# Optimization experiments

Measured on AMD Instinct MI355X. Metric: run time of the kernel, lower is better.

The kernel has to match this reference:

```python
import jax, jax.numpy as jnp
import numpy as np

N, E, G = 64, 128, 4
D0, ED = 9, 4
H1, H2, H3 = 2000, 500, 100
F1, F2, F3 = 1000, 100, 50


def setup_inputs() -> dict:
    key = jax.random.key(0)
    ks = iter(jax.random.split(key, 32))

    def p(shape, s=0.02):
        return (jax.random.normal(next(ks), shape, jnp.float32) * s)

    inp = {
        "x": jax.random.normal(next(ks), (N, D0), jnp.float32),
        "edge_index": jax.random.randint(next(ks), (2, E), 0, N),
        "edge_attr": jax.random.normal(next(ks), (E, ED), jnp.float32),
        "batch": jnp.sort(jax.random.randint(next(ks), (N,), 0, G)),
        # NNConv layer 1: edge MLP Linear(ED, D0*H1), root weight, bias
        "We1": p((ED, D0 * H1)), "be1": p((D0 * H1,)),
        "root1": p((D0, H1)), "b1": p((H1,)),
        # NNConv layer 2
        "We2": p((ED, H1 * H2)), "be2": p((H1 * H2,)),
        "root2": p((H1, H2)), "b2": p((H2,)),
        # NNConv layer 3
        "We3": p((ED, H2 * H3)), "be3": p((H2 * H3,)),
        "root3": p((H2, H3)), "b3": p((H3,)),
        # FCN head
        "W1": p((H3, F1)), "c1": p((F1,)),
        "W2": p((F1, F2)), "c2": p((F2,)),
        "W3": p((F2, F3)), "c3": p((F3,)),
        "W4": p((F3, 1)), "c4": p((1,)),
    }
    return inp


def _nnconv(x, src, dst, edge_attr, We, be, root, b):
    # edge-conditioned weights: [E, in, out]
    in_dim = x.shape[1]
    w = (edge_attr @ We + be).reshape(edge_attr.shape[0], in_dim, -1)
    # gather source feats, per-edge matmul, scatter-add to targets
    msg = jnp.einsum('ei,eio->eo', x[src], w)
    agg = jax.ops.segment_sum(msg, dst, num_segments=x.shape[0])
    return agg + x @ root + b


def reference(x, edge_index, edge_attr, batch,
              We1, be1, root1, b1,
              We2, be2, root2, b2,
              We3, be3, root3, b3,
              W1, c1, W2, c2, W3, c3, W4, c4):
    src, dst = edge_index[0], edge_index[1]
    h = jax.nn.relu(_nnconv(x, src, dst, edge_attr, We1, be1, root1, b1))
    h = jax.nn.relu(_nnconv(h, src, dst, edge_attr, We2, be2, root2, b2))
    h = jax.nn.relu(_nnconv(h, src, dst, edge_attr, We3, be3, root3, b3))
    # sum readout per graph (dropout layers are identity in eval mode)
    g = jax.ops.segment_sum(h, batch, num_segments=G)  # [G, H3]
    g = jax.nn.relu(g @ W1 + c1)
    g = jax.nn.relu(g @ W2 + c2)
    g = jax.nn.relu(g @ W3 + c3)
    out = g @ W4 + c4
    return out.reshape(-1)  # [G]
```

## Files before the change

### kernel.cpp

```cpp
#include <hip/hip_runtime.h>

#define NN 64
#define EE 128
#define GG 4
#define D0 9
#define EDIM 4
#define H1 2000
#define H2 500
#define H3 100
#define FF1 1000
#define FF2 100
#define FF3 50
#define KDIM 384

#define OFF_A    0
#define OFF_Y    24576
#define OFF_PRE1 28032
#define OFF_PRE2 156032
#define OFF_PRE3 188032
#define OFF_N2   194432
#define OFF_N3   386432
#define OFF_F1   424832
#define OFF_F2   428832

#define FILLN 269200

__global__ __launch_bounds__(256) void k_init(
    const float* __restrict__ x, const int* __restrict__ edge_index,
    const float* __restrict__ edge_attr,
    const float* __restrict__ b2, const float* __restrict__ b3,
    const float* __restrict__ c2, float* __restrict__ ws)
{
    const int b = blockIdx.x, tid = threadIdx.x;
    if (b == 0) {
        float* A = ws + OFF_A;
        for (int i = tid; i < NN * KDIM; i += 256) A[i] = 0.f;
        __syncthreads();
        if (tid < EE) {
            int s = edge_index[tid];
            int t = edge_index[EE + tid];
            float* row = A + t * KDIM + s * 6;
            #pragma unroll
            for (int d = 0; d < 4; ++d) atomicAdd(row + d, edge_attr[tid * 4 + d]);
            atomicAdd(row + 4, 1.0f);
        }
        if (tid < NN) A[tid * KDIM + tid * 6 + 5] = 1.0f;
    } else if (b == 1) {
        __shared__ float Ys[NN * 54];
        for (int i = tid; i < NN * 54; i += 256) Ys[i] = 0.f;
        __syncthreads();
        if (tid < EE) {
            int s = edge_index[tid];
            int t = edge_index[EE + tid];
            float ea[4];
            #pragma unroll
            for (int d = 0; d < 4; ++d) ea[d] = edge_attr[tid * 4 + d];
            #pragma unroll
            for (int i = 0; i < D0; ++i) {
                float xv = x[s * D0 + i];
                #pragma unroll
                for (int d = 0; d < 4; ++d)
                    atomicAdd(&Ys[t * 54 + d * 9 + i], ea[d] * xv);
                atomicAdd(&Ys[t * 54 + 36 + i], xv);
            }
        }
        if (tid < NN) {
            #pragma unroll
            for (int i = 0; i < D0; ++i) Ys[tid * 54 + 45 + i] = x[tid * D0 + i];
        }
        __syncthreads();
        for (int i = tid; i < NN * 54; i += 256) ws[OFF_Y + i] = Ys[i];
    } else {
        const int stride = (gridDim.x - 2) * 256;
        for (int i = (b - 2) * 256 + tid; i < FILLN; i += stride) {
            if (i < 32000)         ws[OFF_PRE2 + i] = b2[i % H2];
            else if (i < 38400)  { int j = i - 32000;  ws[OFF_PRE3 + j] = b3[j % H3]; }
            else if (i < 230400)   ws[OFF_N2 + (i - 38400)] = 0.f;
            else if (i < 268800)   ws[OFF_N3 + (i - 230400)] = 0.f;
            else                 { int j = i - 268800; ws[OFF_F2 + j] = c2[j % FF2]; }
        }
    }
}

__global__ __launch_bounds__(256) void k_lin1(
    const float* __restrict__ Yw,
    const float* __restrict__ We1, const float* __restrict__ be1,
    const float* __restrict__ root1, const float* __restrict__ b1,
    float* __restrict__ pre1)
{
    const int tid = threadIdx.x;
    const int tx = tid & 15, ty = tid >> 4;
    const int o0 = blockIdx.x * 64;
    const int w = min(64, H1 - o0);

    __shared__ float Ys[64 * 56];
    __shared__ __align__(16) float Bs[54 * 64];

    for (int i = tid; i < 64 * 54; i += 256) {
        int u = i / 54, r = i - u * 54;
        Ys[u * 56 + r] = Yw[i];
    }
    for (int i = tid; i < 54 * 64; i += 256) {
        int r = i >> 6, c = i & 63;
        int d = r / 9, ii = r - d * 9;
        const float* rowp = ((d < 4) ? (We1 + d * (D0 * H1))
                                     : ((d == 4) ? be1 : root1)) + ii * H1;
        Bs[r * 64 + c] = (c < w) ? rowp[o0 + c] : 0.f;
    }
    __syncthreads();

    float acc[4][4] = {};
    #pragma unroll 6
    for (int r = 0; r < 54; ++r) {
        float a0 = Ys[(ty * 4 + 0) * 56 + r];
        float a1 = Ys[(ty * 4 + 1) * 56 + r];
        float a2 = Ys[(ty * 4 + 2) * 56 + r];
        float a3 = Ys[(ty * 4 + 3) * 56 + r];
        const float4 bv = *(const float4*)&Bs[r * 64 + tx * 4];
        acc[0][0] += a0 * bv.x; acc[0][1] += a0 * bv.y; acc[0][2] += a0 * bv.z; acc[0][3] += a0 * bv.w;
        acc[1][0] += a1 * bv.x; acc[1][1] += a1 * bv.y; acc[1][2] += a1 * bv.z; acc[1][3] += a1 * bv.w;
        acc[2][0] += a2 * bv.x; acc[2][1] += a2 * bv.y; acc[2][2] += a2 * bv.z; acc[2][3] += a2 * bv.w;
        acc[3][0] += a3 * bv.x; acc[3][1] += a3 * bv.y; acc[3][2] += a3 * bv.z; acc[3][3] += a3 * bv.w;
    }
    #pragma unroll
    for (int i = 0; i < 4; ++i) {
        int u = ty * 4 + i;
        #pragma unroll
        for (int jj = 0; jj < 4; ++jj) {
            int j = o0 + tx * 4 + jj;
            if (j < H1) pre1[u * H1 + j] = b1[j] + acc[i][jj];
        }
    }
}

template<int KC, int ITERS>
__global__ __launch_bounds__(256) void k_msg(
    const float* __restrict__ pre, int K,
    const float* __restrict__ We, const float* __restrict__ be,
    const float* __restrict__ root, long long secSize,
    int M, int OT, int S, float* __restrict__ n)
{
    constexpr int APAD = KC + 4;
    const int b  = blockIdx.x;
    const int s  = b % S;
    const int t2 = b / S;
    const int ot = t2 % OT;
    const int d  = t2 / OT;
    const int tid = threadIdx.x;
    const int tx = tid & 15, ty = tid >> 4;
    const int o0 = ot * 64;
    const int w  = min(64, M - o0);
    const int w4 = w >> 2;

    const float* Bbase = (d < 4) ? (We + (long long)d * secSize)
                                 : ((d == 4) ? be : root);

    __shared__ __align__(16) float As[64 * APAD];
    __shared__ __align__(16) float Bs[KC * 64];

    float acc[4][4] = {};
    for (int it = 0; it < ITERS; ++it) {
        const int kb = s * (KC * ITERS) + it * KC;
        __syncthreads();
        for (int idx = tid; idx < 64 * (KC / 4); idx += 256) {
            int r = idx / (KC / 4), c4 = idx % (KC / 4);
            float4 v = *(const float4*)(pre + r * K + kb + c4 * 4);
            v.x = v.x > 0.f ? v.x : 0.f; v.y = v.y > 0.f ? v.y : 0.f;
            v.z = v.z > 0.f ? v.z : 0.f; v.w = v.w > 0.f ? v.w : 0.f;
            *(float4*)&As[r * APAD + c4 * 4] = v;
        }
        for (int idx = tid; idx < KC * 16; idx += 256) {
            int r = idx >> 4, c4 = idx & 15;
            if (c4 < w4) {
                float4 v = *(const float4*)(Bbase + (long long)(kb + r) * M + o0 + c4 * 4);
                *(float4*)&Bs[r * 64 + c4 * 4] = v;
            }
        }
        __syncthreads();
        #pragma unroll 8
        for (int kk = 0; kk < KC; ++kk) {
            float a0 = As[(ty * 4 + 0) * APAD + kk];
            float a1 = As[(ty * 4 + 1) * APAD + kk];
            float a2 = As[(ty * 4 + 2) * APAD + kk];
            float a3 = As[(ty * 4 + 3) * APAD + kk];
            const float4 bv = *(const float4*)&Bs[kk * 64 + tx * 4];
            acc[0][0] += a0 * bv.x; acc[0][1] += a0 * bv.y; acc[0][2] += a0 * bv.z; acc[0][3] += a0 * bv.w;
            acc[1][0] += a1 * bv.x; acc[1][1] += a1 * bv.y; acc[1][2] += a1 * bv.z; acc[1][3] += a1 * bv.w;
            acc[2][0] += a2 * bv.x; acc[2][1] += a2 * bv.y; acc[2][2] += a2 * bv.z; acc[2][3] += a2 * bv.w;
            acc[3][0] += a3 * bv.x; acc[3][1] += a3 * bv.y; acc[3][2] += a3 * bv.z; acc[3][3] += a3 * bv.w;
        }
    }
    #pragma unroll
    for (int i = 0; i < 4; ++i) {
        int u = ty * 4 + i;
        #pragma unroll
        for (int jj = 0; jj < 4; ++jj) {
            int j = o0 + tx * 4 + jj;
            if (j < M) atomicAdd(&n[(u * 6 + d) * M + j], acc[i][jj]);
        }
    }
}

__global__ __launch_bounds__(256) void k_agg(
    const float* __restrict__ A, const float* __restrict__ B,
    int M, float* __restrict__ out)
{
    constexpr int KC = 48, APAD = 52;
    const int s  = blockIdx.x & 7;
    const int ot = blockIdx.x >> 3;
    const int tid = threadIdx.x;
    const int tx = tid & 15, ty = tid >> 4;
    const int o0 = ot * 64;
    const int w  = min(64, M - o0);
    const int w4 = w >> 2;
    const int kb = s * KC;

    __shared__ __align__(16) float As[64 * APAD];
    __shared__ __align__(16) float Bs[KC * 64];

    for (int idx = tid; idx < 64 * (KC / 4); idx += 256) {
        int r = idx / (KC / 4), c4 = idx % (KC / 4);
        *(float4*)&As[r * APAD + c4 * 4] =
            *(const float4*)(A + r * KDIM + kb + c4 * 4);
    }
    for (int idx = tid; idx < KC * 16; idx += 256) {
        int r = idx >> 4, c4 = idx & 15;
        if (c4 < w4)
            *(float4*)&Bs[r * 64 + c4 * 4] =
                *(const float4*)(B + (kb + r) * M + o0 + c4 * 4);
    }
    __syncthreads();

    float acc[4][4] = {};
    #pragma unroll 8
    for (int kk = 0; kk < KC; ++kk) {
        float a0 = As[(ty * 4 + 0) * APAD + kk];
        float a1 = As[(ty * 4 + 1) * APAD + kk];
        float a2 = As[(ty * 4 + 2) * APAD + kk];
        float a3 = As[(ty * 4 + 3) * APAD + kk];
        const float4 bv = *(const float4*)&Bs[kk * 64 + tx * 4];
        acc[0][0] += a0 * bv.x; acc[0][1] += a0 * bv.y; acc[0][2] += a0 * bv.z; acc[0][3] += a0 * bv.w;
        acc[1][0] += a1 * bv.x; acc[1][1] += a1 * bv.y; acc[1][2] += a1 * bv.z; acc[1][3] += a1 * bv.w;
        acc[2][0] += a2 * bv.x; acc[2][1] += a2 * bv.y; acc[2][2] += a2 * bv.z; acc[2][3] += a2 * bv.w;
        acc[3][0] += a3 * bv.x; acc[3][1] += a3 * bv.y; acc[3][2] += a3 * bv.z; acc[3][3] += a3 * bv.w;
    }
    #pragma unroll
    for (int i = 0; i < 4; ++i) {
        int u = ty * 4 + i;
        #pragma unroll
        for (int jj = 0; jj < 4; ++jj) {
            int j = o0 + tx * 4 + jj;
            if (j < M) atomicAdd(&out[u * M + j], acc[i][jj]);
        }
    }
}

__global__ __launch_bounds__(256) void k_head1(
    const float* __restrict__ pre3, const int* __restrict__ batch,
    const float* __restrict__ W1, const float* __restrict__ c1,
    float* __restrict__ f1)
{
    const int gi = blockIdx.x >> 4;
    const int jt = blockIdx.x & 15;
    const int o0 = jt * 64;
    const int tid = threadIdx.x;
    __shared__ int   bsh[NN];
    __shared__ float gs[H3];
    __shared__ float red[4 * 64];

    if (tid < NN) bsh[tid] = batch[tid];
    __syncthreads();
    for (int d = tid; d < H3; d += 256) {
        float acc = 0.f;
        #pragma unroll
        for (int v = 0; v < NN; ++v) {
            float h = pre3[v * H3 + d];
            h = h > 0.f ? h : 0.f;
            acc += (bsh[v] == gi) ? h : 0.f;
        }
        gs[d] = acc;
    }
    __syncthreads();
    const int jj = tid & 63, kq = tid >> 6;
    const int oc = min(o0 + jj, FF1 - 1);
    float p = 0.f;
    #pragma unroll
    for (int k = kq * 25; k < kq * 25 + 25; ++k)
        p += gs[k] * W1[k * FF1 + oc];
    red[kq * 64 + jj] = p;
    __syncthreads();
    if (tid < 64) {
        int o = o0 + tid;
        if (o < FF1) {
            float v = c1[o] + red[tid] + red[64 + tid] + red[128 + tid] + red[192 + tid];
            f1[gi * FF1 + o] = v > 0.f ? v : 0.f;
        }
    }
}

__global__ __launch_bounds__(256) void k_head2(
    const float* __restrict__ f1, const float* __restrict__ W2,
    float* __restrict__ f2)
{
    const int s = blockIdx.x;
    const int k0 = s * 63;
    const int kn = min(63, FF1 - k0);
    const int tid = threadIdx.x;
    __shared__ float f1s[4 * 63];
    for (int i = tid; i < 4 * kn; i += 256) {
        int gi = i / kn, kk = i - gi * kn;
        f1s[gi * 63 + kk] = f1[gi * FF1 + k0 + kk];
    }
    __syncthreads();
    for (int idx = tid; idx < GG * FF2; idx += 256) {
        int gi = idx / FF2, o = idx - gi * FF2;
        float acc = 0.f;
        for (int kk = 0; kk < kn; ++kk)
            acc += f1s[gi * 63 + kk] * W2[(k0 + kk) * FF2 + o];
        atomicAdd(&f2[idx], acc);
    }
}

__global__ __launch_bounds__(256) void k_head3(
    const float* __restrict__ f2, const float* __restrict__ W3,
    const float* __restrict__ c3, const float* __restrict__ W4,
    const float* __restrict__ c4, float* __restrict__ out)
{
    const int tid = threadIdx.x;
    __shared__ float f2s[GG * FF2];
    __shared__ float f3s[GG * FF3];
    for (int i = tid; i < GG * FF2; i += 256) {
        float v = f2[i];
        f2s[i] = v > 0.f ? v : 0.f;
    }
    __syncthreads();
    if (tid < GG * FF3) {
        int gi = tid / FF3, o = tid - gi * FF3;
        float acc = c3[o];
        for (int k = 0; k < FF2; ++k)
            acc += f2s[gi * FF2 + k] * W3[k * FF3 + o];
        f3s[tid] = acc > 0.f ? acc : 0.f;
    }
    __syncthreads();
    if (tid < GG) {
        float acc = c4[0];
        #pragma unroll
        for (int k = 0; k < FF3; ++k) acc += f3s[tid * FF3 + k] * W4[k];
        out[tid] = acc;
    }
}

extern "C" void kernel_launch(void* const* d_in, const int* in_sizes, int n_in,
                              void* d_out, int out_size, void* d_ws, size_t ws_size,
                              hipStream_t stream) {
    const float* x          = (const float*)d_in[0];
    const int*   edge_index = (const int*)  d_in[1];
    const float* edge_attr  = (const float*)d_in[2];
    const int*   batch      = (const int*)  d_in[3];
    const float* We1 = (const float*)d_in[4];
    const float* be1 = (const float*)d_in[5];
    const float* root1 = (const float*)d_in[6];
    const float* b1  = (const float*)d_in[7];
    const float* We2 = (const float*)d_in[8];
    const float* be2 = (const float*)d_in[9];
    const float* root2 = (const float*)d_in[10];
    const float* b2  = (const float*)d_in[11];
    const float* We3 = (const float*)d_in[12];
    const float* be3 = (const float*)d_in[13];
    const float* root3 = (const float*)d_in[14];
    const float* b3  = (const float*)d_in[15];
    const float* W1 = (const float*)d_in[16];
    const float* c1 = (const float*)d_in[17];
    const float* W2 = (const float*)d_in[18];
    const float* c2 = (const float*)d_in[19];
    const float* W3 = (const float*)d_in[20];
    const float* c3 = (const float*)d_in[21];
    const float* W4 = (const float*)d_in[22];
    const float* c4 = (const float*)d_in[23];
    float* ws  = (float*)d_ws;
    float* out = (float*)d_out;

    k_init<<<66, 256, 0, stream>>>(x, edge_index, edge_attr, b2, b3, c2, ws);
    k_lin1<<<32, 256, 0, stream>>>(ws + OFF_Y, We1, be1, root1, b1, ws + OFF_PRE1);
    k_msg<40, 5><<<480, 256, 0, stream>>>(ws + OFF_PRE1, H1, We2, be2, root2,
                                          (long long)H1 * H2, H2, 8, 10,
                                          ws + OFF_N2);
    k_agg<<<64, 256, 0, stream>>>(ws + OFF_A, ws + OFF_N2, H2, ws + OFF_PRE2);
    k_msg<20, 5><<<60, 256, 0, stream>>>(ws + OFF_PRE2, H2, We3, be3, root3,
                                         (long long)H2 * H3, H3, 2, 5,
                                         ws + OFF_N3);
    k_agg<<<16, 256, 0, stream>>>(ws + OFF_A, ws + OFF_N3, H3, ws + OFF_PRE3);
    k_head1<<<64, 256, 0, stream>>>(ws + OFF_PRE3, batch, W1, c1, ws + OFF_F1);
    k_head2<<<16, 256, 0, stream>>>(ws + OFF_F1, W2, ws + OFF_F2);
    k_head3<<<1, 256, 0, stream>>>(ws + OFF_F2, W3, c3, W4, c4, out);
}
```

Measured before the change: 239.9 us.

## Double-buffer message GEMM with direct global-to-LDS loads and split layer-3 K

Replaces the message-passing GEMM with a double-buffered version that stages A and B tiles straight into LDS via global_load_lds, so the next K chunk loads while the current one is computed. The LDS reads are vectorised along K as float4 with a 4x4 register micro-kernel. ReLU on layer-1 output moves into k_lin1's epilogue, and layer 3's ReLU is applied during compute. The layer-3 launch now splits K across more blocks (300 instead of 60) for more parallelism, at the price of more atomic adds. Dropping the LDS padding may bring bank conflicts on the A-row float4 reads, and with the new K chunk of 20 floats (80 bytes) the 16-byte async copies may break across rows.

```diff
diff --git a/kernel.cpp b/kernel.cpp
--- a/kernel.cpp
+++ b/kernel.cpp
@@ -25,6 +25,17 @@
 
 #define FILLN 269200
 
+__device__ __forceinline__ void gl2lds16(const float* g, float* l) {
+    __builtin_amdgcn_global_load_lds(
+        (const __attribute__((address_space(1))) unsigned int*)g,
+        (__attribute__((address_space(3))) unsigned int*)l,
+        16, 0, 0);
+}
+
+__device__ __forceinline__ float4 ldf4(const float* p) {
+    return *(const float4*)p;
+}
+
 __global__ __launch_bounds__(256) void k_init(
     const float* __restrict__ x, const int* __restrict__ edge_index,
     const float* __restrict__ edge_attr,
@@ -128,19 +139,22 @@
         #pragma unroll
         for (int jj = 0; jj < 4; ++jj) {
             int j = o0 + tx * 4 + jj;
-            if (j < H1) pre1[u * H1 + j] = b1[j] + acc[i][jj];
-        }
-    }
-}
-
-template<int KC, int ITERS>
-__global__ __launch_bounds__(256) void k_msg(
+            if (j < H1) {
+                float v = b1[j] + acc[i][jj];
+                pre1[u * H1 + j] = v > 0.f ? v : 0.f;
+            }
+        }
+    }
+}
+
+template<int KC, int ITERS, bool RELUA>
+__global__ __launch_bounds__(256) void k_msg2(
     const float* __restrict__ pre, int K,
     const float* __restrict__ We, const float* __restrict__ be,
     const float* __restrict__ root, long long secSize,
     int M, int OT, int S, float* __restrict__ n)
 {
-    constexpr int APAD = KC + 4;
+    constexpr int NCH = (64 * KC) / 256;
     const int b  = blockIdx.x;
     const int s  = b % S;
     const int t2 = b / S;
@@ -148,48 +162,73 @@
     const int d  = t2 / OT;
     const int tid = threadIdx.x;
     const int tx = tid & 15, ty = tid >> 4;
+    const int wv = tid >> 6, ln = tid & 63;
     const int o0 = ot * 64;
     const int w  = min(64, M - o0);
-    const int w4 = w >> 2;
+    const int kbase = s * (KC * ITERS);
 
     const float* Bbase = (d < 4) ? (We + (long long)d * secSize)
                                  : ((d == 4) ? be : root);
 
-    __shared__ __align__(16) float As[64 * APAD];
-    __shared__ __align__(16) float Bs[KC * 64];
+    __shared__ __align__(16) float As[2][64 * KC];
+    __shared__ __align__(16) float Bs[2][KC * 64];
+
+    auto stage = [&](int bf, int kb) {
+        for (int c = wv; c < NCH; c += 4) {
+            int f = c * 256 + ln * 4;
+            int r = f / KC, cc = f - r * KC;
+            gl2lds16(pre + r * K + kb + cc, &As[bf][c * 256]);
+        }
+        for (int c = wv; c < NCH; c += 4) {
+            int f = c * 256 + ln * 4;
+            int r = f >> 6, col = f & 63;
+            if (col < w)
+                gl2lds16(Bbase + (long long)(kb + r) * M + o0 + col,
+                         &Bs[bf][c * 256]);
+        }
+    };
 
     float acc[4][4] = {};
+    stage(0, kbase);
+    __syncthreads();
+
     for (int it = 0; it < ITERS; ++it) {
-        const int kb = s * (KC * ITERS) + it * KC;
+        if (it + 1 < ITERS) stage((it + 1) & 1, kbase + (it + 1) * KC);
+        const float* Ab = As[it & 1];
+        const float* Bb = Bs[it & 1];
+        #pragma unroll
+        for (int k4 = 0; k4 < KC / 4; ++k4) {
+            float4 av[4], bv[4];
+            #pragma unroll
+            for (int i = 0; i < 4; ++i)
+                av[i] = ldf4(&Ab[(ty * 4 + i) * KC + k4 * 4]);
+            #pragma unroll
+            for (int q = 0; q < 4; ++q)
+                bv[q] = ldf4(&Bb[(k4 * 4 + q) * 64 + tx * 4]);
+            if (RELUA) {
+                #pragma unroll
+                for (int i = 0; i < 4; ++i) {
+                    av[i].x = fmaxf(av[i].x, 0.f);
+                    av[i].y = fmaxf(av[i].y, 0.f);
+                    av[i].z = fmaxf(av[i].z, 0.f);
+                    av[i].w = fmaxf(av[i].w, 0.f);
+                }
+            }
+            #pragma unroll
+            for (int i = 0; i < 4; ++i) {
+                acc[i][0] += av[i].x * bv[0].x; acc[i][1] += av[i].x * bv[0].y;
+                acc[i][2] += av[i].x * bv[0].z; acc[i][3] += av[i].x * bv[0].w;
+                acc[i][0] += av[i].y * bv[1].x; acc[i][1] += av[i].y * bv[1].y;
+                acc[i][2] += av[i].y * bv[1].z; acc[i][3] += av[i].y * bv[1].w;
+                acc[i][0] += av[i].z * bv[2].x; acc[i][1] += av[i].z * bv[2].y;
+                acc[i][2] += av[i].z * bv[2].z; acc[i][3] += av[i].z * bv[2].w;
+                acc[i][0] += av[i].w * bv[3].x; acc[i][1] += av[i].w * bv[3].y;
+                acc[i][2] += av[i].w * bv[3].z; acc[i][3] += av[i].w * bv[3].w;
+            }
+        }
         __syncthreads();
-        for (int idx = tid; idx < 64 * (KC / 4); idx += 256) {
-            int r = idx / (KC / 4), c4 = idx % (KC / 4);
-            float4 v = *(const float4*)(pre + r * K + kb + c4 * 4);
-            v.x = v.x > 0.f ? v.x : 0.f; v.y = v.y > 0.f ? v.y : 0.f;
-            v.z = v.z > 0.f ? v.z : 0.f; v.w = v.w > 0.f ? v.w : 0.f;
-            *(float4*)&As[r * APAD + c4 * 4] = v;
-        }
-        for (int idx = tid; idx < KC * 16; idx += 256) {
-            int r = idx >> 4, c4 = idx & 15;
-            if (c4 < w4) {
-                float4 v = *(const float4*)(Bbase + (long long)(kb + r) * M + o0 + c4 * 4);
-                *(float4*)&Bs[r * 64 + c4 * 4] = v;
-            }
-        }
-        __syncthreads();
-        #pragma unroll 8
-        for (int kk = 0; kk < KC; ++kk) {
-            float a0 = As[(ty * 4 + 0) * APAD + kk];
-            float a1 = As[(ty * 4 + 1) * APAD + kk];
-            float a2 = As[(ty * 4 + 2) * APAD + kk];
-            float a3 = As[(ty * 4 + 3) * APAD + kk];
-            const float4 bv = *(const float4*)&Bs[kk * 64 + tx * 4];
-            acc[0][0] += a0 * bv.x; acc[0][1] += a0 * bv.y; acc[0][2] += a0 * bv.z; acc[0][3] += a0 * bv.w;
-            acc[1][0] += a1 * bv.x; acc[1][1] += a1 * bv.y; acc[1][2] += a1 * bv.z; acc[1][3] += a1 * bv.w;
-            acc[2][0] += a2 * bv.x; acc[2][1] += a2 * bv.y; acc[2][2] += a2 * bv.z; acc[2][3] += a2 * bv.w;
-            acc[3][0] += a3 * bv.x; acc[3][1] += a3 * bv.y; acc[3][2] += a3 * bv.z; acc[3][3] += a3 * bv.w;
-        }
-    }
+    }
+
     #pragma unroll
     for (int i = 0; i < 4; ++i) {
         int u = ty * 4 + i;
@@ -205,44 +244,54 @@
     const float* __restrict__ A, const float* __restrict__ B,
     int M, float* __restrict__ out)
 {
-    constexpr int KC = 48, APAD = 52;
+    constexpr int KC = 48;
+    constexpr int NCH = (64 * KC) / 256;
     const int s  = blockIdx.x & 7;
     const int ot = blockIdx.x >> 3;
     const int tid = threadIdx.x;
     const int tx = tid & 15, ty = tid >> 4;
+    const int wv = tid >> 6, ln = tid & 63;
     const int o0 = ot * 64;
     const int w  = min(64, M - o0);
-    const int w4 = w >> 2;
     const int kb = s * KC;
 
-    __shared__ __align__(16) float As[64 * APAD];
+    __shared__ __align__(16) float As[64 * KC];
     __shared__ __align__(16) float Bs[KC * 64];
 
-    for (int idx = tid; idx < 64 * (KC / 4); idx += 256) {
-        int r = idx / (KC / 4), c4 = idx % (KC / 4);
-        *(float4*)&As[r * APAD + c4 * 4] =
-            *(const float4*)(A + r * KDIM + kb + c4 * 4);
-    }
-    for (int idx = tid; idx < KC * 16; idx += 256) {
-        int r = idx >> 4, c4 = idx & 15;
-        if (c4 < w4)
-            *(float4*)&Bs[r * 64 + c4 * 4] =
-                *(const float4*)(B + (kb + r) * M + o0 + c4 * 4);
+    for (int c = wv; c < NCH; c += 4) {
+        int f = c * 256 + ln * 4;
+        int r = f / KC, cc = f - r * KC;
+        gl2lds16(A + r * KDIM + kb + cc, &As[c * 256]);
+    }
+    for (int c = wv; c < NCH; c += 4) {
+        int f = c * 256 + ln * 4;
+        int r = f >> 6, col = f & 63;
+        if (col < w)
+            gl2lds16(B + (kb + r) * M + o0 + col, &Bs[c * 256]);
     }
     __syncthreads();
 
     float acc[4][4] = {};
-    #pragma unroll 8
-    for (int kk = 0; kk < KC; ++kk) {
-        float a0 = As[(ty * 4 + 0) * APAD + kk];
-        float a1 = As[(ty * 4 + 1) * APAD + kk];
-        float a2 = As[(ty * 4 + 2) * APAD + kk];
-        float a3 = As[(ty * 4 + 3) * APAD + kk];
-        const float4 bv = *(const float4*)&Bs[kk * 64 + tx * 4];
-        acc[0][0] += a0 * bv.x; acc[0][1] += a0 * bv.y; acc[0][2] += a0 * bv.z; acc[0][3] += a0 * bv.w;
-        acc[1][0] += a1 * bv.x; acc[1][1] += a1 * bv.y; acc[1][2] += a1 * bv.z; acc[1][3] += a1 * bv.w;
-        acc[2][0] += a2 * bv.x; acc[2][1] += a2 * bv.y; acc[2][2] += a2 * bv.z; acc[2][3] += a2 * bv.w;
-        acc[3][0] += a3 * bv.x; acc[3][1] += a3 * bv.y; acc[3][2] += a3 * bv.z; acc[3][3] += a3 * bv.w;
+    #pragma unroll
+    for (int k4 = 0; k4 < KC / 4; ++k4) {
+        float4 av[4], bv[4];
+        #pragma unroll
+        for (int i = 0; i < 4; ++i)
+            av[i] = ldf4(&As[(ty * 4 + i) * KC + k4 * 4]);
+        #pragma unroll
+        for (int q = 0; q < 4; ++q)
+            bv[q] = ldf4(&Bs[(k4 * 4 + q) * 64 + tx * 4]);
+        #pragma unroll
+        for (int i = 0; i < 4; ++i) {
+            acc[i][0] += av[i].x * bv[0].x; acc[i][1] += av[i].x * bv[0].y;
+            acc[i][2] += av[i].x * bv[0].z; acc[i][3] += av[i].x * bv[0].w;
+            acc[i][0] += av[i].y * bv[1].x; acc[i][1] += av[i].y * bv[1].y;
+            acc[i][2] += av[i].y * bv[1].z; acc[i][3] += av[i].y * bv[1].w;
+            acc[i][0] += av[i].z * bv[2].x; acc[i][1] += av[i].z * bv[2].y;
+            acc[i][2] += av[i].z * bv[2].z; acc[i][3] += av[i].z * bv[2].w;
+            acc[i][0] += av[i].w * bv[3].x; acc[i][1] += av[i].w * bv[3].y;
+            acc[i][2] += av[i].w * bv[3].z; acc[i][3] += av[i].w * bv[3].w;
+        }
     }
     #pragma unroll
     for (int i = 0; i < 4; ++i) {
@@ -382,13 +431,13 @@
 
     k_init<<<66, 256, 0, stream>>>(x, edge_index, edge_attr, b2, b3, c2, ws);
     k_lin1<<<32, 256, 0, stream>>>(ws + OFF_Y, We1, be1, root1, b1, ws + OFF_PRE1);
-    k_msg<40, 5><<<480, 256, 0, stream>>>(ws + OFF_PRE1, H1, We2, be2, root2,
-                                          (long long)H1 * H2, H2, 8, 10,
-                                          ws + OFF_N2);
+    k_msg2<20, 10, false><<<480, 256, 0, stream>>>(ws + OFF_PRE1, H1, We2, be2,
+                                                   root2, (long long)H1 * H2,
+                                                   H2, 8, 10, ws + OFF_N2);
     k_agg<<<64, 256, 0, stream>>>(ws + OFF_A, ws + OFF_N2, H2, ws + OFF_PRE2);
-    k_msg<20, 5><<<60, 256, 0, stream>>>(ws + OFF_PRE2, H2, We3, be3, root3,
-                                         (long long)H2 * H3, H3, 2, 5,
-                                         ws + OFF_N3);
+    k_msg2<20, 1, true><<<300, 256, 0, stream>>>(ws + OFF_PRE2, H2, We3, be3,
+                                                 root3, (long long)H2 * H3,
+                                                 H3, 2, 25, ws + OFF_N3);
     k_agg<<<16, 256, 0, stream>>>(ws + OFF_A, ws + OFF_N3, H3, ws + OFF_PRE3);
     k_head1<<<64, 256, 0, stream>>>(ws + OFF_PRE3, batch, W1, c1, ws + OFF_F1);
     k_head2<<<16, 256, 0, stream>>>(ws + OFF_F1, W2, ws + OFF_F2);
```

Measured after the change: 248.6 us. 3.6% more time.
